# Kernel optimization log

Hardware: AMD Instinct MI355X
Metric: run time of the kernel (lower is better)

## Reference

```python
import jax, jax.numpy as jnp
import numpy as np

B, N, F, FOBS, D = 4, 1024, 128, 32, 128
K_HOP = 3  # os.environ k_hop default 3


def setup_inputs() -> dict:
    key = jax.random.key(0)
    k0, k1, k2, k3, k4 = jax.random.split(key, 5)
    X = jax.random.normal(k0, (B, N, F), jnp.float32)
    # xavier-ish scales for params
    a_link = jax.random.normal(k1, (FOBS, 1), jnp.float32) * (1.414 / np.sqrt(FOBS + 1))
    W0 = jax.random.normal(k2, (F, D), jnp.float32) * np.sqrt(2.0 / (F + D))
    W1 = jax.random.normal(k3, (D, D), jnp.float32) * np.sqrt(1.0 / D)
    W2 = jax.random.normal(k4, (D, D), jnp.float32) * np.sqrt(1.0 / D)
    return {"X": X, "a_link": a_link, "W0": W0, "W1": W1, "W2": W2}


def reference(X, a_link, W0, W1, W2):
    eye = jnp.eye(N, dtype=X.dtype)

    def per_graph(Xb):  # Xb: [N, F]
        h = Xb[:, :FOBS]                                   # [N, FOBS]
        # e_ij = a_link^T |h_i - h_j|
        e = jnp.einsum('ijf,fo->ij', jnp.abs(h[:, None, :] - h[None, :, :]), a_link)
        A = jax.nn.sigmoid(e)
        A = A * (1.0 - eye)                                # zero diagonal (A - diag(diag(A)))
        Dm = jnp.zeros_like(A)                             # diag(diag(A)) is zero after removal
        A_hat = A + eye
        d_inv_sqrt = jnp.sum(A_hat, axis=1) ** -0.5        # row sums (dim=1 in mini_batch path)
        norm = d_inv_sqrt[:, None] * A_hat * d_inv_sqrt[None, :]  # D^-1/2 A_hat D^-1/2
        H = norm @ (Xb @ W0)                               # k = 0
        for Wk in (W1, W2):                                # k = 1 .. K_HOP-1 (norm detached in torch)
            H = jax.lax.stop_gradient(norm) @ (H @ Wk)
        return jax.nn.relu(H), A, Dm

    Hs, As, Ds = jax.vmap(per_graph)(X)
    return Hs, As, X, Ds
```

## Files before the change

kernel.cpp:

```cpp
#include <hip/hip_runtime.h>
#include <math.h>

#define BB 4
#define NN 1024
#define FF 128
#define DD 128
#define FOBS 32

typedef __attribute__((ext_vector_type(8))) short bfrag;
typedef __attribute__((ext_vector_type(4))) float ffrag;
typedef __attribute__((ext_vector_type(4))) unsigned short us4;

__device__ __forceinline__ unsigned short f2bf(float x) {
    unsigned u = __builtin_bit_cast(unsigned, x);
    u += 0x7fffu + ((u >> 16) & 1u);
    return (unsigned short)(u >> 16);
}
__device__ __forceinline__ float bf2f(unsigned short s) {
    unsigned u = (unsigned)s << 16;
    return __builtin_bit_cast(float, u);
}
__device__ __forceinline__ void gload16(const void* g, void* l) {
    __builtin_amdgcn_global_load_lds((const __attribute__((address_space(1))) unsigned*)g,
                                     (__attribute__((address_space(3))) unsigned*)l, 16, 0, 0);
}

__global__ __launch_bounds__(256) void zero_f4(float4* __restrict__ p, int n4) {
    int i = blockIdx.x * 256 + threadIdx.x;
    if (i < n4) p[i] = make_float4(0.f, 0.f, 0.f, 0.f);
}

__global__ __launch_bounds__(256) void adj_kernel(const float* __restrict__ X,
                                                  const float* __restrict__ a_link,
                                                  const float* __restrict__ W0,
                                                  const float* __restrict__ W1,
                                                  const float* __restrict__ W2,
                                                  float* __restrict__ As,
                                                  unsigned short* __restrict__ Abf,
                                                  unsigned short* __restrict__ Xbf,
                                                  unsigned short* __restrict__ W01t,
                                                  unsigned short* __restrict__ W2t,
                                                  float* __restrict__ Pp,
                                                  float* __restrict__ Xo,
                                                  float* __restrict__ Zd) {
    int tid = threadIdx.x;
    if (blockIdx.z == 5) {
        if (Zd) {
            int q = blockIdx.y * 16 + blockIdx.x;
            float4* Z = (float4*)Zd;
#pragma unroll
            for (int p = 0; p < 16; p++)
                Z[(size_t)q * 4096 + p * 256 + tid] = make_float4(0.f, 0.f, 0.f, 0.f);
        }
        return;
    }
    if (blockIdx.z == 4) {
        int q = (blockIdx.y * 16 + blockIdx.x) * 256 + tid;
        if (q < 16384) {
            int g = q >> 7, f = q & 127;
            float s = 0.f;
            for (int h = 0; h < 128; h++) s += W0[f * 128 + h] * W1[h * 128 + g];
            W01t[q] = f2bf(s);
        } else if (q < 32768) {
            int e = q - 16384;
            int f2 = e >> 7, g = e & 127;
            W2t[e] = f2bf(W2[g * 128 + f2]);
        } else {
            int u = q - 32768;
#pragma unroll
            for (int p = 0; p < 4; p++) {
                size_t i4 = (size_t)u + (size_t)p * 32768;
                float4 v = *(const float4*)&X[i4 * 4];
                us4 o; o[0] = f2bf(v.x); o[1] = f2bf(v.y); o[2] = f2bf(v.z); o[3] = f2bf(v.w);
                *(us4*)&Xbf[i4 * 4] = o;
            }
        }
        return;
    }
    int b = blockIdx.z, i0 = blockIdx.y * 64, j0 = blockIdx.x * 64;
    __shared__ float hi[64][FOBS + 1];
    __shared__ float hj[64][FOBS + 1];
    __shared__ float av[FOBS];
    __shared__ float part_s[64][16];
    const float* Xb = X + (size_t)b * NN * FF;
    if (j0 == 0) {
#pragma unroll
        for (int p = 0; p < 8; p++) {
            int c = p * 256 + tid, r = c >> 5, qq = c & 31;
            *(float4*)&Xo[((size_t)b * NN + i0 + r) * FF + qq * 4] =
                *(const float4*)&Xb[(size_t)(i0 + r) * FF + qq * 4];
        }
    }
#pragma unroll
    for (int l = 0; l < 8; l++) {
        int idx = l * 256 + tid;
        int r = idx >> 5, f = idx & 31;
        hi[r][f] = Xb[(size_t)(i0 + r) * FF + f];
        hj[r][f] = Xb[(size_t)(j0 + r) * FF + f];
    }
    if (tid < FOBS) av[tid] = a_link[tid];
    __syncthreads();

    int ty = tid >> 4, tx = tid & 15;
    int ir = ty * 4, jc = tx * 4;
    float acc[4][4] = {};
#pragma unroll
    for (int f = 0; f < FOBS; f++) {
        float a = av[f];
        float x[4], y[4];
#pragma unroll
        for (int r = 0; r < 4; r++) x[r] = hi[ir + r][f];
#pragma unroll
        for (int c = 0; c < 4; c++) y[c] = hj[jc + c][f];
#pragma unroll
        for (int r = 0; r < 4; r++)
#pragma unroll
            for (int c = 0; c < 4; c++)
                acc[r][c] += fabsf(x[r] - y[c]) * a;
    }
    float* Ab = As + (size_t)b * NN * NN;
    unsigned short* Abb = Abf + (size_t)b * NN * NN;
#pragma unroll
    for (int r = 0; r < 4; r++) {
        int gi = i0 + ir + r;
        float vv[4]; float rs = 0.f;
#pragma unroll
        for (int c = 0; c < 4; c++) {
            int gj = j0 + jc + c;
            float sg = 1.f / (1.f + __expf(-acc[r][c]));
            vv[c] = (gi == gj) ? 0.f : sg;
            rs += vv[c];
        }
        *(float4*)&Ab[(size_t)gi * NN + (j0 + jc)] = make_float4(vv[0], vv[1], vv[2], vv[3]);
        us4 o; o[0] = f2bf(vv[0]); o[1] = f2bf(vv[1]); o[2] = f2bf(vv[2]); o[3] = f2bf(vv[3]);
        *(us4*)&Abb[(size_t)gi * NN + (j0 + jc)] = o;
        part_s[ir + r][tx] = rs;
    }
    __syncthreads();
    if (tid < 64) {
        float s = 0.f;
#pragma unroll
        for (int k = 0; k < 16; k++) s += part_s[tid][k];
        Pp[((size_t)b * NN + i0 + tid) * 16 + blockIdx.x] = s;
    }
}

__global__ __launch_bounds__(256) void t0_kernel(const unsigned short* __restrict__ Xbf,
                                                 const unsigned short* __restrict__ W01t,
                                                 const unsigned short* __restrict__ W2t,
                                                 const float* __restrict__ Pp,
                                                 unsigned short* __restrict__ TtX) {
    int bid = blockIdx.x;
    int b = bid >> 6, n0 = (bid & 63) * 16;
    __shared__ unsigned short W01s[128 * 128];
    __shared__ unsigned short W2s[128 * 128];
    __shared__ unsigned short Xps[16 * 128];
    __shared__ unsigned short Ps[16 * 128];
    __shared__ float dinv_s[16];
    int tid = threadIdx.x;
    const unsigned short* Xb = Xbf + (size_t)b * NN * DD;
    {
        int r = tid >> 4, p = tid & 15;
        float s = Pp[((size_t)b * NN + n0 + r) * 16 + p];
        s += __shfl_xor(s, 1);
        s += __shfl_xor(s, 2);
        s += __shfl_xor(s, 4);
        s += __shfl_xor(s, 8);
        if (p == 0) dinv_s[r] = rsqrtf(1.f + s);
    }
#pragma unroll
    for (int p = 0; p < 8; p++) {
        int c = p * 256 + tid, row = c >> 4, kc = c & 15;
        gload16(W01t + (size_t)row * 128 + ((kc ^ (row & 7)) * 8), W01s + (size_t)c * 8);
    }
#pragma unroll
    for (int p = 0; p < 8; p++) {
        int c = p * 256 + tid, row = c >> 4, kc = c & 15;
        gload16(W2t + (size_t)row * 128 + ((kc ^ (row & 7)) * 8), W2s + (size_t)c * 8);
    }
    {
        int c = tid, row = c >> 4, kc = c & 15;
        gload16(Xb + (size_t)(n0 + row) * 128 + ((kc ^ (row & 7)) * 8), Xps + (size_t)c * 8);
    }
    __syncthreads();

    int w = tid >> 6, l = tid & 63, lr = l & 15, lg = l >> 4;
    ffrag pacc[2] = {};
#pragma unroll
    for (int ks = 0; ks < 4; ks++) {
        int k0 = ks * 32 + lg * 8;
        bfrag a[2], bb;
#pragma unroll
        for (int rb = 0; rb < 2; rb++) {
            int row = w * 32 + rb * 16 + lr;
            int byt = (row * 256 + k0 * 2) ^ ((row & 7) << 4);
            a[rb] = *(const bfrag*)((const char*)W01s + byt);
        }
        {
            int byt = (lr * 256 + k0 * 2) ^ ((lr & 7) << 4);
            bb = *(const bfrag*)((const char*)Xps + byt);
        }
#pragma unroll
        for (int rb = 0; rb < 2; rb++)
            pacc[rb] = __builtin_amdgcn_mfma_f32_16x16x32_bf16(a[rb], bb, pacc[rb], 0, 0, 0);
    }
#pragma unroll
    for (int rb = 0; rb < 2; rb++) {
        int g0 = w * 32 + rb * 16 + lg * 4;
        us4 o;
#pragma unroll
        for (int r = 0; r < 4; r++) o[r] = f2bf(pacc[rb][r]);
        int byt = (lr * 256 + g0 * 2) ^ ((lr & 7) << 4);
        *(us4*)((char*)Ps + byt) = o;
    }
    __syncthreads();
    ffrag tacc[2] = {};
#pragma unroll
    for (int ks = 0; ks < 4; ks++) {
        int k0 = ks * 32 + lg * 8;
        bfrag a2[2], b2;
#pragma unroll
        for (int rb = 0; rb < 2; rb++) {
            int row = w * 32 + rb * 16 + lr;
            int byt = (row * 256 + k0 * 2) ^ ((row & 7) << 4);
            a2[rb] = *(const bfrag*)((const char*)W2s + byt);
        }
        {
            int byt = (lr * 256 + k0 * 2) ^ ((lr & 7) << 4);
            b2 = *(const bfrag*)((const char*)Ps + byt);
        }
#pragma unroll
        for (int rb = 0; rb < 2; rb++)
            tacc[rb] = __builtin_amdgcn_mfma_f32_16x16x32_bf16(a2[rb], b2, tacc[rb], 0, 0, 0);
    }
    unsigned short* Tb = TtX + (size_t)b * DD * NN;
    float dv = dinv_s[lr];
#pragma unroll
    for (int rb = 0; rb < 2; rb++)
#pragma unroll
        for (int r = 0; r < 4; r++) {
            int f2 = w * 32 + rb * 16 + lg * 4 + r;
            Tb[(size_t)f2 * NN + n0 + lr] = f2bf(tacc[rb][r] * dv);
        }
}

template <int LAST>
__global__ __launch_bounds__(256) void ga_kernel(const unsigned short* __restrict__ Abf,
                                                 const float* __restrict__ Pp,
                                                 const unsigned short* __restrict__ Tin,
                                                 unsigned short* __restrict__ Tout,
                                                 float* __restrict__ HsF) {
    int bid = blockIdx.x;
    int fh = bid & 1, panel = bid >> 1;
    int b = panel >> 6, n0 = (panel & 63) * 16;
    __shared__ unsigned short T_s[3 * 64 * 64];
    __shared__ unsigned short A_s[3 * 16 * 64];
    __shared__ float dinv_s[16];
    int tid = threadIdx.x;
    const unsigned short* TbF = Tin + (size_t)b * DD * NN;
    const unsigned short* Tb  = TbF + (size_t)fh * 64 * NN;
    const unsigned short* Ab  = Abf + (size_t)b * NN * NN;

    {
        int r = tid >> 4, p = tid & 15;
        float s = Pp[((size_t)b * NN + n0 + r) * 16 + p];
        s += __shfl_xor(s, 1);
        s += __shfl_xor(s, 2);
        s += __shfl_xor(s, 4);
        s += __shfl_xor(s, 8);
        if (p == 0) dinv_s[r] = rsqrtf(1.f + s);
    }
    auto stageT = [&](int buf, int kt) {
#pragma unroll
        for (int p = 0; p < 2; p++) {
            int c = p * 256 + tid, row = c >> 3, kc = c & 7;
            gload16(Tb + (size_t)row * NN + kt + ((kc ^ (row & 7)) * 8),
                    T_s + (size_t)buf * (64 * 64) + (size_t)c * 8);
        }
        int c = tid & 127, row = c >> 3, kc = c & 7;
        gload16(Ab + (size_t)(n0 + row) * NN + kt + ((kc ^ (row & 7)) * 8),
                A_s + (size_t)buf * (16 * 64) + (size_t)c * 8);
    };
    stageT(0, 0);
    stageT(1, 64);

    int w = tid >> 6, l = tid & 63, lr = l & 15, lg = l >> 4;
    ffrag acc = {};
    int cur = 0, sb = 2;
    for (int t = 0; t < 16; t++) {
        if (t <= 13) stageT(sb, (t + 2) * 64);
        if (t < 14)       asm volatile("s_waitcnt vmcnt(6)" ::: "memory");
        else if (t == 14) asm volatile("s_waitcnt vmcnt(3)" ::: "memory");
        else              asm volatile("s_waitcnt vmcnt(0)" ::: "memory");
        __builtin_amdgcn_s_barrier();
        asm volatile("" ::: "memory");
        const unsigned short* Tc = T_s + (size_t)cur * (64 * 64);
        const unsigned short* Ac = A_s + (size_t)cur * (16 * 64);
#pragma unroll
        for (int ks = 0; ks < 2; ks++) {
            int k0 = ks * 32 + lg * 8;
            bfrag a, bb;
            {
                int row = w * 16 + lr;
                int byt = (row * 128 + k0 * 2) ^ ((row & 7) << 4);
                a = *(const bfrag*)((const char*)Tc + byt);
            }
            {
                int byt = (lr * 128 + k0 * 2) ^ ((lr & 7) << 4);
                bb = *(const bfrag*)((const char*)Ac + byt);
            }
            acc = __builtin_amdgcn_mfma_f32_16x16x32_bf16(a, bb, acc, 0, 0, 0);
        }
        asm volatile("s_waitcnt lgkmcnt(0)" ::: "memory");
        __builtin_amdgcn_s_barrier();
        cur = (cur == 2) ? 0 : cur + 1;
        sb = (sb == 2) ? 0 : sb + 1;
    }

    int nl = lr;
    float dv = dinv_s[nl];
    int f0 = fh * 64 + w * 16 + lg * 4;
    if (LAST) {
        float v[4];
#pragma unroll
        for (int r = 0; r < 4; r++) {
            float idv = bf2f(TbF[(size_t)(f0 + r) * NN + n0 + nl]);
            v[r] = fmaxf((acc[r] + idv) * dv, 0.f);
        }
        *(float4*)&HsF[((size_t)b * NN + n0 + nl) * DD + f0] = make_float4(v[0], v[1], v[2], v[3]);
    } else {
        float dv2 = dv * dv;
        unsigned short* Ob = Tout + (size_t)b * DD * NN;
#pragma unroll
        for (int r = 0; r < 4; r++) {
            float idv = bf2f(TbF[(size_t)(f0 + r) * NN + n0 + nl]);
            Ob[(size_t)(f0 + r) * NN + n0 + nl] = f2bf((acc[r] + idv) * dv2);
        }
    }
}

extern "C" void kernel_launch(void* const* d_in, const int* in_sizes, int n_in,
                              void* d_out, int out_size, void* d_ws, size_t ws_size,
                              hipStream_t stream) {
    const float* X      = (const float*)d_in[0];
    const float* a_link = (const float*)d_in[1];
    const float* W0     = (const float*)d_in[2];
    const float* W1     = (const float*)d_in[3];
    const float* W2     = (const float*)d_in[4];
    float* out = (float*)d_out;

    const size_t HND = (size_t)BB * NN * DD;
    const size_t HNN = (size_t)BB * NN * NN;
    float* Hs = out;
    float* As = out + HND;
    float* Xo = out + HND + HNN;
    float* Ds = out + 2 * HND + HNN;

    const size_t NEED = 11862016;
    bool usews = (ws_size >= NEED);
    char* scr = usews ? (char*)d_ws : (char*)Ds;

    unsigned short* Abf  = (unsigned short*)(scr);
    unsigned short* Xbf  = (unsigned short*)(scr + 8388608);
    unsigned short* TtX  = (unsigned short*)(scr + 9437184);
    unsigned short* TtY  = (unsigned short*)(scr + 10485760);
    unsigned short* W01t = (unsigned short*)(scr + 11534336);
    unsigned short* W2t  = (unsigned short*)(scr + 11567104);
    float* Pp            = (float*)(scr + 11599872);

    adj_kernel<<<dim3(16, 16, usews ? 6 : 5), 256, 0, stream>>>(
        X, a_link, W0, W1, W2, As, Abf, Xbf, W01t, W2t, Pp, Xo, usews ? Ds : nullptr);
    t0_kernel<<<dim3(256), 256, 0, stream>>>(Xbf, W01t, W2t, Pp, TtX);
    ga_kernel<0><<<dim3(512), 256, 0, stream>>>(Abf, Pp, TtX, TtY, nullptr);
    ga_kernel<0><<<dim3(512), 256, 0, stream>>>(Abf, Pp, TtY, TtX, nullptr);
    ga_kernel<1><<<dim3(512), 256, 0, stream>>>(Abf, Pp, TtX, nullptr, Hs);

    if (!usews)
        zero_f4<<<dim3(4096), 256, 0, stream>>>((float4*)Ds, (int)(HNN / 4));
}
```

Measured before the change: 50.54 us.

## Exploit adjacency symmetry with triangular tiles and widen GA k-tile to 128

The adjacency kernel now launches only upper-triangular 64x64 tile pairs (136 per batch) and writes each off-diagonal tile plus its transpose via shared memory, computing both row and column partial sums, which halves the |h_i-h_j| compute. The zero-fill and weight-prep side jobs are re-indexed for the smaller grid. Separately, the graph-aggregation GEMM stages 128-wide K tiles (8 iterations instead of 16) with deeper waits, cutting barriers at the cost of more LDS per block. Transposed stores are less coalesced, and the adjacency kernel's cost is largely bound by writing A in fp32 and bf16, so the compute saving may matter less.

Result: slower. 54.15 us (+7.2%).

```diff
diff --git a/kernel.cpp b/kernel.cpp
--- a/kernel.cpp
+++ b/kernel.cpp
@@ -10,6 +10,8 @@
 typedef __attribute__((ext_vector_type(8))) short bfrag;
 typedef __attribute__((ext_vector_type(4))) float ffrag;
 typedef __attribute__((ext_vector_type(4))) unsigned short us4;
+
+#define NTRI 136
 
 __device__ __forceinline__ unsigned short f2bf(float x) {
     unsigned u = __builtin_bit_cast(unsigned, x);
@@ -46,44 +48,57 @@
     int tid = threadIdx.x;
     if (blockIdx.z == 5) {
         if (Zd) {
-            int q = blockIdx.y * 16 + blockIdx.x;
             float4* Z = (float4*)Zd;
 #pragma unroll
-            for (int p = 0; p < 16; p++)
-                Z[(size_t)q * 4096 + p * 256 + tid] = make_float4(0.f, 0.f, 0.f, 0.f);
+            for (int it = 0; it < 31; it++) {
+                int i = it * (NTRI * 256) + blockIdx.x * 256 + tid;
+                if (i < 1048576) Z[i] = make_float4(0.f, 0.f, 0.f, 0.f);
+            }
         }
         return;
     }
     if (blockIdx.z == 4) {
-        int q = (blockIdx.y * 16 + blockIdx.x) * 256 + tid;
-        if (q < 16384) {
-            int g = q >> 7, f = q & 127;
-            float s = 0.f;
-            for (int h = 0; h < 128; h++) s += W0[f * 128 + h] * W1[h * 128 + g];
-            W01t[q] = f2bf(s);
-        } else if (q < 32768) {
-            int e = q - 16384;
-            int f2 = e >> 7, g = e & 127;
-            W2t[e] = f2bf(W2[g * 128 + f2]);
-        } else {
-            int u = q - 32768;
-#pragma unroll
-            for (int p = 0; p < 4; p++) {
-                size_t i4 = (size_t)u + (size_t)p * 32768;
-                float4 v = *(const float4*)&X[i4 * 4];
-                us4 o; o[0] = f2bf(v.x); o[1] = f2bf(v.y); o[2] = f2bf(v.z); o[3] = f2bf(v.w);
-                *(us4*)&Xbf[i4 * 4] = o;
+        for (int it = 0; it < 2; it++) {
+            int q = it * (NTRI * 256) + blockIdx.x * 256 + tid;
+            if (q >= 65536) break;
+            if (q < 16384) {
+                int g = q >> 7, f = q & 127;
+                float s = 0.f;
+                for (int h = 0; h < 128; h++) s += W0[f * 128 + h] * W1[h * 128 + g];
+                W01t[q] = f2bf(s);
+            } else if (q < 32768) {
+                int e = q - 16384;
+                int f2 = e >> 7, g = e & 127;
+                W2t[e] = f2bf(W2[g * 128 + f2]);
+            } else {
+                int u = q - 32768;
+#pragma unroll
+                for (int p = 0; p < 4; p++) {
+                    size_t i4 = (size_t)u + (size_t)p * 32768;
+                    float4 v = *(const float4*)&X[i4 * 4];
+                    us4 o; o[0] = f2bf(v.x); o[1] = f2bf(v.y); o[2] = f2bf(v.z); o[3] = f2bf(v.w);
+                    *(us4*)&Xbf[i4 * 4] = o;
+                }
             }
         }
         return;
     }
-    int b = blockIdx.z, i0 = blockIdx.y * 64, j0 = blockIdx.x * 64;
+    int b = blockIdx.z;
+    int t = blockIdx.x;
+    int ta = 0, rem = t;
+    while (rem >= 16 - ta) { rem -= 16 - ta; ta++; }
+    int tb = ta + rem;
+    int i0 = ta * 64, j0 = tb * 64;
+    bool diag = (ta == tb);
+
     __shared__ float hi[64][FOBS + 1];
     __shared__ float hj[64][FOBS + 1];
     __shared__ float av[FOBS];
-    __shared__ float part_s[64][16];
+    __shared__ float part_r[64][16];
+    __shared__ float part_c[64][16];
+    __shared__ float st[64][68];
     const float* Xb = X + (size_t)b * NN * FF;
-    if (j0 == 0) {
+    if (diag) {
 #pragma unroll
         for (int p = 0; p < 8; p++) {
             int c = p * 256 + tid, r = c >> 5, qq = c & 31;
@@ -120,6 +135,7 @@
     }
     float* Ab = As + (size_t)b * NN * NN;
     unsigned short* Abb = Abf + (size_t)b * NN * NN;
+    float cs[4] = {0.f, 0.f, 0.f, 0.f};
 #pragma unroll
     for (int r = 0; r < 4; r++) {
         int gi = i0 + ir + r;
@@ -134,14 +150,39 @@
         *(float4*)&Ab[(size_t)gi * NN + (j0 + jc)] = make_float4(vv[0], vv[1], vv[2], vv[3]);
         us4 o; o[0] = f2bf(vv[0]); o[1] = f2bf(vv[1]); o[2] = f2bf(vv[2]); o[3] = f2bf(vv[3]);
         *(us4*)&Abb[(size_t)gi * NN + (j0 + jc)] = o;
-        part_s[ir + r][tx] = rs;
+        part_r[ir + r][tx] = rs;
+        if (!diag) {
+#pragma unroll
+            for (int c = 0; c < 4; c++) { st[jc + c][ir + r] = vv[c]; cs[c] += vv[c]; }
+        }
+    }
+    if (!diag) {
+#pragma unroll
+        for (int c = 0; c < 4; c++) part_c[jc + c][ty] = cs[c];
     }
     __syncthreads();
     if (tid < 64) {
         float s = 0.f;
 #pragma unroll
-        for (int k = 0; k < 16; k++) s += part_s[tid][k];
-        Pp[((size_t)b * NN + i0 + tid) * 16 + blockIdx.x] = s;
+        for (int k = 0; k < 16; k++) s += part_r[tid][k];
+        Pp[((size_t)b * NN + i0 + tid) * 16 + tb] = s;
+    }
+    if (!diag) {
+#pragma unroll
+        for (int r2 = 0; r2 < 4; r2++) {
+            int jl = ty * 4 + r2;
+            int gj = j0 + jl;
+            float4 v4 = *(const float4*)&st[jl][tx * 4];
+            *(float4*)&Ab[(size_t)gj * NN + (i0 + tx * 4)] = v4;
+            us4 o; o[0] = f2bf(v4.x); o[1] = f2bf(v4.y); o[2] = f2bf(v4.z); o[3] = f2bf(v4.w);
+            *(us4*)&Abb[(size_t)gj * NN + (i0 + tx * 4)] = o;
+        }
+        if (tid < 64) {
+            float s = 0.f;
+#pragma unroll
+            for (int k = 0; k < 16; k++) s += part_c[tid][k];
+            Pp[((size_t)b * NN + j0 + tid) * 16 + ta] = s;
+        }
     }
 }
 
@@ -253,8 +294,8 @@
     int bid = blockIdx.x;
     int fh = bid & 1, panel = bid >> 1;
     int b = panel >> 6, n0 = (panel & 63) * 16;
-    __shared__ unsigned short T_s[3 * 64 * 64];
-    __shared__ unsigned short A_s[3 * 16 * 64];
+    __shared__ unsigned short T_s[3 * 64 * 128];
+    __shared__ unsigned short A_s[3 * 16 * 128];
     __shared__ float dinv_s[16];
     int tid = threadIdx.x;
     const unsigned short* TbF = Tin + (size_t)b * DD * NN;
@@ -272,41 +313,41 @@
     }
     auto stageT = [&](int buf, int kt) {
 #pragma unroll
-        for (int p = 0; p < 2; p++) {
-            int c = p * 256 + tid, row = c >> 3, kc = c & 7;
+        for (int p = 0; p < 4; p++) {
+            int c = p * 256 + tid, row = c >> 4, kc = c & 15;
             gload16(Tb + (size_t)row * NN + kt + ((kc ^ (row & 7)) * 8),
-                    T_s + (size_t)buf * (64 * 64) + (size_t)c * 8);
-        }
-        int c = tid & 127, row = c >> 3, kc = c & 7;
+                    T_s + (size_t)buf * (64 * 128) + (size_t)c * 8);
+        }
+        int c = tid, row = c >> 4, kc = c & 15;
         gload16(Ab + (size_t)(n0 + row) * NN + kt + ((kc ^ (row & 7)) * 8),
-                A_s + (size_t)buf * (16 * 64) + (size_t)c * 8);
+                A_s + (size_t)buf * (16 * 128) + (size_t)c * 8);
     };
     stageT(0, 0);
-    stageT(1, 64);
+    stageT(1, 128);
 
     int w = tid >> 6, l = tid & 63, lr = l & 15, lg = l >> 4;
     ffrag acc = {};
     int cur = 0, sb = 2;
-    for (int t = 0; t < 16; t++) {
-        if (t <= 13) stageT(sb, (t + 2) * 64);
-        if (t < 14)       asm volatile("s_waitcnt vmcnt(6)" ::: "memory");
-        else if (t == 14) asm volatile("s_waitcnt vmcnt(3)" ::: "memory");
-        else              asm volatile("s_waitcnt vmcnt(0)" ::: "memory");
+    for (int tt = 0; tt < 8; tt++) {
+        if (tt <= 5) stageT(sb, (tt + 2) * 128);
+        if (tt < 6)       asm volatile("s_waitcnt vmcnt(10)" ::: "memory");
+        else if (tt == 6) asm volatile("s_waitcnt vmcnt(5)"  ::: "memory");
+        else              asm volatile("s_waitcnt vmcnt(0)"  ::: "memory");
         __builtin_amdgcn_s_barrier();
         asm volatile("" ::: "memory");
-        const unsigned short* Tc = T_s + (size_t)cur * (64 * 64);
-        const unsigned short* Ac = A_s + (size_t)cur * (16 * 64);
-#pragma unroll
-        for (int ks = 0; ks < 2; ks++) {
+        const unsigned short* Tc = T_s + (size_t)cur * (64 * 128);
+        const unsigned short* Ac = A_s + (size_t)cur * (16 * 128);
+#pragma unroll
+        for (int ks = 0; ks < 4; ks++) {
             int k0 = ks * 32 + lg * 8;
             bfrag a, bb;
             {
                 int row = w * 16 + lr;
-                int byt = (row * 128 + k0 * 2) ^ ((row & 7) << 4);
+                int byt = (row * 256 + k0 * 2) ^ ((row & 7) << 4);
                 a = *(const bfrag*)((const char*)Tc + byt);
             }
             {
-                int byt = (lr * 128 + k0 * 2) ^ ((lr & 7) << 4);
+                int byt = (lr * 256 + k0 * 2) ^ ((lr & 7) << 4);
                 bb = *(const bfrag*)((const char*)Ac + byt);
             }
             acc = __builtin_amdgcn_mfma_f32_16x16x32_bf16(a, bb, acc, 0, 0, 0);
@@ -368,7 +409,7 @@
     unsigned short* W2t  = (unsigned short*)(scr + 11567104);
     float* Pp            = (float*)(scr + 11599872);
 
-    adj_kernel<<<dim3(16, 16, usews ? 6 : 5), 256, 0, stream>>>(
+    adj_kernel<<<dim3(NTRI, 1, usews ? 6 : 5), 256, 0, stream>>>(
         X, a_link, W0, W1, W2, As, Abf, Xbf, W01t, W2t, Pp, Xo, usews ? Ds : nullptr);
     t0_kernel<<<dim3(256), 256, 0, stream>>>(Xbf, W01t, W2t, Pp, TtX);
     ga_kernel<0><<<dim3(512), 256, 0, stream>>>(Abf, Pp, TtX, TtY, nullptr);
```
